# Performance work log

Measured on AMD Instinct MI355X. Metric: run time of the kernel, lower is better.

The kernel has to match this reference:

```python
import jax, jax.numpy as jnp
import numpy as np

B, C, H, W = 4, 256, 48, 48
KD, NH, AR = 32, 8, 4
D = AR * KD            # 128, value dim per head
NHKD = NH * KD         # 256
DH = NH * D            # 1024
EPS = 1e-5


def _bn(y, g, b):
    # BN with fresh running stats (mean=0, var=1): y*g/sqrt(1+eps)+b, over channel dim
    s = g / jnp.sqrt(jnp.float32(1.0) + EPS)
    return y * s[None, :, None] + b[None, :, None]


def setup_inputs() -> dict:
    key = jax.random.key(0)
    ks = jax.random.split(key, 13)
    w = lambda k, sh: jax.random.normal(k, sh, jnp.float32) * 0.05
    g = lambda k, sh: 1.0 + jax.random.normal(k, sh, jnp.float32) * 0.05
    return {
        "x": jax.random.normal(ks[0], (B, C, H, W), jnp.float32),
        "wq": w(ks[1], (NHKD, C)), "gq": g(ks[2], (NHKD,)), "bq": w(ks[3], (NHKD,)),
        "wk": w(ks[4], (NHKD, C)), "gk": g(ks[5], (NHKD,)), "bk": w(ks[6], (NHKD,)),
        "wv": w(ks[7], (DH, C)),   "gv": g(ks[8], (DH,)),   "bv": w(ks[9], (DH,)),
        "wp": w(ks[10], (C, DH)),  "gp": g(ks[11], (C,)),   "bp": w(ks[12], (C,)),
    }


def reference(x, wq, gq, bq, wk, gk, bk, wv, gv, bv, wp, gp, bp):
    b, c, h, w = x.shape
    n = h * w
    xf = x.reshape(b, c, n)                                   # [B,C,N]
    # 1x1 conv == channel matmul, then BN
    q = _bn(jnp.einsum('oc,bcn->bon', wq, xf), gq, bq).reshape(b, NH, KD, n)
    k = _bn(jnp.einsum('oc,bcn->bon', wk, xf), gk, bk).reshape(b, NH, KD, n)
    v = _bn(jnp.einsum('oc,bcn->bon', wv, xf), gv, bv).reshape(b, NH, D, n)
    # NOTE: original forward does NOT apply self.scale
    attn = jax.nn.softmax(jnp.einsum('bhkn,bhkm->bhnm', q, k), axis=-1)  # [B,H,N,N]
    xx = jnp.einsum('bhnm,bhdm->bhdn', attn, v).reshape(b, DH, n)        # [B,DH,N]
    out = _bn(jnp.einsum('oc,bcn->bon', wp, jax.nn.relu(xx)), gp, bp)
    return out.reshape(b, c, h, w)
```

## Files before the change

kernel.cpp:

```cpp
#include <hip/hip_runtime.h>

#define BB 4
#define C 256
#define HW 2304
#define NH 8
#define KD 32
#define D 128
#define DH 1024
#define MQ 256

typedef unsigned short bf16u;
typedef __attribute__((ext_vector_type(8))) short short8;
typedef __attribute__((ext_vector_type(4))) float f32x4;
typedef __attribute__((ext_vector_type(4))) unsigned ux4;
typedef __attribute__((ext_vector_type(2))) unsigned ux2;

union U8 { ux4 u; short8 s; };

__device__ __forceinline__ bf16u f2b(float f) {
    unsigned u = __float_as_uint(f);
    return (bf16u)((u + 0x7fffu + ((u >> 16) & 1u)) >> 16);
}
__device__ __forceinline__ unsigned pkb(float a, float b) {
    return __builtin_amdgcn_perm(__float_as_uint(b) + 0x8000u,
                                 __float_as_uint(a) + 0x8000u, 0x07060302u);
}

__device__ __forceinline__ void glds16(const bf16u* g, bf16u* l) {
    __builtin_amdgcn_global_load_lds(
        (const __attribute__((address_space(1))) unsigned int*)g,
        (__attribute__((address_space(3))) unsigned int*)l,
        16, 0, 0);
}

#define MFMA32 __builtin_amdgcn_mfma_f32_16x16x32_bf16

__global__ __launch_bounds__(256) void prepx(
    const float* __restrict__ wq, const float* __restrict__ wk, const float* __restrict__ wv,
    const float* __restrict__ gq, const float* __restrict__ bq,
    const float* __restrict__ gk, const float* __restrict__ bk,
    const float* __restrict__ gv, const float* __restrict__ bv,
    const float* __restrict__ x,
    bf16u* __restrict__ WcT, float* __restrict__ biasc, bf16u* __restrict__ xT)
{
    __shared__ float tile[64][68];
    const float rs = rsqrtf(1.0f + 1e-5f);
    const float L2E = 1.4426950408889634f;
    const int t = threadIdx.x, blk = blockIdx.x;
    if (blk < 192) {
        const int idx = (blk*256 + t) * 8;
        const int row = idx >> 8;
        const int k   = idx & 255;
        const float* src; float sc;
        if (row < 256)      { src = wq + idx;            sc = gq[row]*rs*L2E; }
        else if (row < 512) { src = wk + (idx - 65536);  sc = gk[row-256]*rs; }
        else                { src = wv + (idx - 131072); sc = gv[row-512]*rs; }
        float4 a = *(const float4*)(src);
        float4 c = *(const float4*)(src + 4);
        ux4 v;
        v.x = pkb(a.x*sc, a.y*sc); v.y = pkb(a.z*sc, a.w*sc);
        v.z = pkb(c.x*sc, c.y*sc); v.w = pkb(c.z*sc, c.w*sc);
        const size_t dst = (size_t)((row>>7)*8 + (k>>5))*4096
                         + (size_t)((row&127)*4 + ((k&31)>>3))*8;
        *(ux4*)(WcT + dst) = v;
    } else if (blk == 192) {
        #pragma unroll
        for (int kk = 0; kk < 6; ++kk) {
            const int r = kk*256 + t;
            float v;
            if (r < 256)      v = bq[r] * L2E;
            else if (r < 512) v = bk[r - 256];
            else              v = bv[r - 512];
            biasc[r] = v;
        }
    } else {
        const int idx = blk - 193;
        const int c0 = (idx & 3) * 64, n0 = ((idx >> 2) % 36) * 64, b = idx / 144;
        const float* xb = x + (size_t)b * C * HW;
        #pragma unroll
        for (int rr = 0; rr < 4; ++rr) {
            const int cl = rr*16 + (t >> 4);
            float4 v = *(const float4*)(xb + (size_t)(c0 + cl) * HW + n0 + (t & 15)*4);
            tile[cl][(t&15)*4+0] = v.x; tile[cl][(t&15)*4+1] = v.y;
            tile[cl][(t&15)*4+2] = v.z; tile[cl][(t&15)*4+3] = v.w;
        }
        __syncthreads();
        const int nl = t >> 2, ch = t & 3;
        short8 v0, v1;
        #pragma unroll
        for (int kk = 0; kk < 8; ++kk) v0[kk] = (short)f2b(tile[ch*16+kk][nl]);
        #pragma unroll
        for (int kk = 0; kk < 8; ++kk) v1[kk] = (short)f2b(tile[ch*16+8+kk][nl]);
        bf16u* dst = xT + ((size_t)b*HW + n0 + nl) * C + c0 + ch*16;
        *(short8*)(dst)     = v0;
        *(short8*)(dst + 8) = v1;
    }
}

__global__ __launch_bounds__(256, 3) void qkv_gemm(
    const bf16u* __restrict__ WcT, const float* __restrict__ biasc,
    const bf16u* __restrict__ xT,
    bf16u* __restrict__ qT, bf16u* __restrict__ kT, bf16u* __restrict__ vO)
{
    const int mt = blockIdx.x, ntb = blockIdx.y, b = blockIdx.z;
    const int r0 = mt * 128, c0 = ntb * 128;
    const int t = threadIdx.x, w = t >> 6, l = t & 63;
    const int l15 = l & 15, q = l >> 4;
    const int wr = w >> 1, wc = w & 1;

    __shared__ bf16u smem[24576];

    const bf16u* xb = xT + (size_t)b * HW * C;

    const int sA0 = w*128 + l, sA1 = w*128 + 64 + l;
    const bf16u* gA0 = WcT + (size_t)mt*32768 + (size_t)sA0*8;
    const bf16u* gA1 = WcT + (size_t)mt*32768 + (size_t)sA1*8;
    const bf16u* gB0 = xb + (size_t)(c0 + (sA0>>2)) * C + (sA0&3)*8;
    const bf16u* gB1 = xb + (size_t)(c0 + (sA1>>2)) * C + (sA1&3)*8;

    f32x4 acc[4][4];
    #pragma unroll
    for (int i = 0; i < 4; ++i)
        #pragma unroll
        for (int j = 0; j < 4; ++j) { acc[i][j][0]=0.f; acc[i][j][1]=0.f; acc[i][j][2]=0.f; acc[i][j][3]=0.f; }

    auto stage = [&](int it2, int bb) {
        bf16u* As = smem + bb*4096;
        bf16u* Bs = smem + 12288 + bb*4096;
        glds16(gA0 + it2*4096, As + sA0*8);
        glds16(gA1 + it2*4096, As + sA1*8);
        glds16(gB0 + it2*32,   Bs + sA0*8);
        glds16(gB1 + it2*32,   Bs + sA1*8);
    };

    const bool isV = (r0 >= 512);
    stage(0, 0); stage(1, 1);
    for (int it = 0; it < 8; ++it) {
        __syncthreads();
        if (it + 2 < 8) stage(it + 2, (it + 2) % 3);
        const bf16u* A = smem + (it % 3) * 4096;
        const bf16u* B = smem + 12288 + (it % 3) * 4096;
        short8 af[4], bf[4];
        #pragma unroll
        for (int i = 0; i < 4; ++i) af[i] = *(const short8*)(A + (wr*64 + i*16 + l15)*32 + q*8);
        #pragma unroll
        for (int j = 0; j < 4; ++j) bf[j] = *(const short8*)(B + (wc*64 + j*16 + l15)*32 + q*8);
        if (!isV) {
            #pragma unroll
            for (int i = 0; i < 4; ++i)
                #pragma unroll
                for (int j = 0; j < 4; ++j)
                    acc[i][j] = MFMA32(af[i], bf[j], acc[i][j], 0, 0, 0);
        } else {
            #pragma unroll
            for (int i = 0; i < 4; ++i)
                #pragma unroll
                for (int j = 0; j < 4; ++j)
                    acc[i][j] = MFMA32(bf[j], af[i], acc[i][j], 0, 0, 0);
        }
    }

    __syncthreads();
    bf16u* Od = smem + w * 4608;

    if (!isV) {
        float bC[4][4];
        #pragma unroll
        for (int i = 0; i < 4; ++i)
            #pragma unroll
            for (int r = 0; r < 4; ++r)
                bC[i][r] = biasc[r0 + wr*64 + i*16 + q*4 + r];
        #pragma unroll
        for (int i = 0; i < 4; ++i)
            #pragma unroll
            for (int j = 0; j < 4; ++j) {
                float y0 = acc[i][j][0] + bC[i][0];
                float y1 = acc[i][j][1] + bC[i][1];
                float y2 = acc[i][j][2] + bC[i][2];
                float y3 = acc[i][j][3] + bC[i][3];
                ux2 pk; pk.x = pkb(y0, y1); pk.y = pkb(y2, y3);
                *(ux2*)(Od + (j*16 + l15)*72 + i*16 + q*4) = pk;
            }
        bf16u* dst = (r0 < 256) ? qT : kT;
        #pragma unroll
        for (int hh = 0; hh < 2; ++hh) {
            const int h = ((r0 & 255) + wr*64 + hh*32) >> 5;
            bf16u* dh_ = dst + (size_t)(b*NH + h) * HW * KD;
            #pragma unroll
            for (int rg = 0; rg < 4; ++rg) {
                const int row = rg*16 + (l >> 2);
                const int n = c0 + wc*64 + row;
                short8 v = *(const short8*)(Od + row*72 + hh*32 + (l & 3)*8);
                *(short8*)(dh_ + (size_t)n * KD + (l & 3)*8) = v;
            }
        }
    } else {
        float bC[4];
        #pragma unroll
        for (int i = 0; i < 4; ++i)
            bC[i] = biasc[r0 + wr*64 + i*16 + l15];
        #pragma unroll
        for (int i = 0; i < 4; ++i)
            #pragma unroll
            for (int j = 0; j < 4; ++j) {
                float y0 = acc[i][j][0] + bC[i];
                float y1 = acc[i][j][1] + bC[i];
                float y2 = acc[i][j][2] + bC[i];
                float y3 = acc[i][j][3] + bC[i];
                ux2 pk; pk.x = pkb(y0, y1); pk.y = pkb(y2, y3);
                const int p = (j >> 1)*32 + q*8 + (j & 1)*4;
                *(ux2*)(Od + (i*16 + l15)*72 + p) = pk;
            }
        bf16u* dst = vO + (size_t)b * DH * HW;
        #pragma unroll
        for (int it2 = 0; it2 < 8; ++it2) {
            const int row = it2*8 + (l >> 3);
            const int d = (r0 - 512) + wr*64 + row;
            short8 v = *(const short8*)(Od + row*72 + (l & 7)*8);
            *(short8*)(dst + (size_t)d * HW + c0 + wc*64 + (l & 7)*8) = v;
        }
    }
}

__global__ __launch_bounds__(128, 2) void attn_mfma(
    const bf16u* __restrict__ qT, const bf16u* __restrict__ kT,
    const bf16u* __restrict__ vg, bf16u* __restrict__ xg)
{
    const int nt = blockIdx.x, h = blockIdx.y, b = blockIdx.z;
    const int n0 = nt * 96;
    const int t = threadIdx.x;
    const int w = t >> 6, l = t & 63, l15 = l & 15, q = l >> 4;

    const bf16u* qTh = qT + (size_t)(b*NH + h) * HW * KD;
    const bf16u* kTh = kT + (size_t)(b*NH + h) * HW * KD;
    const bf16u* vh  = vg + ((size_t)b*DH + (size_t)h*D) * HW;

    __shared__ bf16u smem[16384];

    short8 qf[3];
    #pragma unroll
    for (int g = 0; g < 3; ++g)
        qf[g] = *(const short8*)(qTh + (size_t)(n0 + w*48 + g*16 + l15) * KD + q*8);

    const short8 ones = { (short)0x3F80, (short)0x3F80, (short)0x3F80, (short)0x3F80,
                          (short)0x3F80, (short)0x3F80, (short)0x3F80, (short)0x3F80 };

    f32x4 o[3][8];
    #pragma unroll
    for (int g = 0; g < 3; ++g)
        #pragma unroll
        for (int d = 0; d < 8; ++d) { o[g][d][0]=0.f; o[g][d][1]=0.f; o[g][d][2]=0.f; o[g][d][3]=0.f; }
    f32x4 os[3];
    #pragma unroll
    for (int g = 0; g < 3; ++g) { os[g][0]=0.f; os[g][1]=0.f; os[g][2]=0.f; os[g][3]=0.f; }
    const f32x4 zero = {0.f, 0.f, 0.f, 0.f};

    auto stageV = [&](int m0, int bb) {
        bf16u* Vs = smem + bb*8192;
        #pragma unroll
        for (int j = 0; j < 8; ++j) {
            const int s = (w*8 + j)*64 + l;
            const int d = s >> 3, c = s & 7, cg = c ^ (d & 7);
            glds16(vh + (size_t)d*HW + m0 + cg*8, Vs + (w*8 + j)*512);
        }
    };

    short8 kfc[4];
    #pragma unroll
    for (int kt = 0; kt < 4; ++kt)
        kfc[kt] = *(const short8*)(kTh + (size_t)(kt*16 + l15) * KD + q*8);
    stageV(0, 0);

    for (int mt = 0; mt < 36; ++mt) {
        __syncthreads();
        if (mt < 35) stageV((mt+1)*64, (mt+1)&1);
        const bf16u* Vs = smem + (mt&1)*8192;

        unsigned dA[3][4], dB[3][4];
        #pragma unroll
        for (int g = 0; g < 3; ++g) {
            f32x4 st[4];
            #pragma unroll
            for (int kt = 0; kt < 4; ++kt)
                st[kt] = MFMA32(kfc[kt], qf[g], zero, 0, 0, 0);
            #pragma unroll
            for (int kt = 0; kt < 4; ++kt) {
                float p0 = __builtin_amdgcn_exp2f(st[kt][0]);
                float p1 = __builtin_amdgcn_exp2f(st[kt][1]);
                float p2 = __builtin_amdgcn_exp2f(st[kt][2]);
                float p3 = __builtin_amdgcn_exp2f(st[kt][3]);
                dA[g][kt] = pkb(p0, p1); dB[g][kt] = pkb(p2, p3);
            }
        }

        if (mt < 35) {
            #pragma unroll
            for (int kt = 0; kt < 4; ++kt)
                kfc[kt] = *(const short8*)(kTh + (size_t)((mt+1)*64 + kt*16 + l15) * KD + q*8);
        }

        #pragma unroll
        for (int kh = 0; kh < 2; ++kh) {
            U8 u[3];
            #pragma unroll
            for (int g = 0; g < 3; ++g) {
                u[g].u[0] = dA[g][kh*2];   u[g].u[1] = dB[g][kh*2];
                u[g].u[2] = dA[g][kh*2+1]; u[g].u[3] = dB[g][kh*2+1];
            }
            #pragma unroll
            for (int dt = 0; dt < 8; ++dt) {
                const int d = dt*16 + l15;
                short8 vf = *(const short8*)(Vs + d*64 + (((kh*4 + q) ^ (d & 7)) * 8));
                #pragma unroll
                for (int g = 0; g < 3; ++g)
                    o[g][dt] = MFMA32(u[g].s, vf, o[g][dt], 0, 0, 0);
            }
            #pragma unroll
            for (int g = 0; g < 3; ++g)
                os[g] = MFMA32(u[g].s, ones, os[g], 0, 0, 0);
        }
    }

    float inv[3][4];
    #pragma unroll
    for (int g = 0; g < 3; ++g)
        #pragma unroll
        for (int r = 0; r < 4; ++r)
            inv[g][r] = 1.0f / os[g][r];
    __syncthreads();
    bf16u* Od = smem + w * 6528;
    #pragma unroll
    for (int g = 0; g < 3; ++g)
        #pragma unroll
        for (int dt = 0; dt < 8; ++dt)
            #pragma unroll
            for (int r = 0; r < 4; ++r) {
                float v = fmaxf(o[g][dt][r] * inv[g][r], 0.f);
                Od[(g*16 + q*4 + r)*136 + dt*16 + l15] = f2b(v);
            }
    bf16u* xb = xg + ((size_t)b*HW + n0 + w*48) * DH + h*D;
    #pragma unroll
    for (int it = 0; it < 6; ++it) {
        const int row = it*8 + (l >> 3);
        #pragma unroll
        for (int hf = 0; hf < 2; ++hf) {
            const int ch = hf*8 + (l & 7);
            *(short8*)(xb + (size_t)row*DH + ch*8) =
                *(const short8*)(Od + row*136 + ch*8);
        }
    }
}

__global__ __launch_bounds__(256) void prep2(
    const float* __restrict__ wp, const float* __restrict__ gp,
    bf16u* __restrict__ WpT)
{
    const float rs = rsqrtf(1.0f + 1e-5f);
    const int item = blockIdx.x*256 + threadIdx.x;
    const int row = item >> 7;
    const int k   = (item & 127) * 8;
    const float sc = gp[row] * rs;
    const float* src = wp + (size_t)row*DH + k;
    float4 a = *(const float4*)(src);
    float4 c = *(const float4*)(src + 4);
    ux4 v;
    v.x = pkb(a.x*sc, a.y*sc); v.y = pkb(a.z*sc, a.w*sc);
    v.z = pkb(c.x*sc, c.y*sc); v.w = pkb(c.z*sc, c.w*sc);
    const size_t dst = (size_t)((row>>4)*32 + (k>>5))*512
                     + (size_t)(((k>>3)&3)*16 + (row&15))*8;
    *(ux4*)(WpT + dst) = v;
}

__global__ __launch_bounds__(256, 3) void out_gemm(
    const bf16u* __restrict__ WpT, const float* __restrict__ bp,
    const bf16u* __restrict__ xx, float* __restrict__ out)
{
    const int mt = blockIdx.x, ntb = blockIdx.y, b = blockIdx.z;
    const int r0 = mt * 64, c0 = ntb * 64;
    const int t = threadIdx.x, w = t >> 6, l = t & 63;
    const int l15 = l & 15, q = l >> 4;
    const int wr = w >> 1, wc = w & 1;

    __shared__ bf16u smem[12288];

    const bf16u* xb = xx + (size_t)b * HW * DH;

    const int sB0 = w*128 + l, sB1 = w*128 + 64 + l;
    const bf16u* gB0 = xb + (size_t)(c0 + (sB0>>3)) * DH + (sB0&7)*8;
    const bf16u* gB1 = xb + (size_t)(c0 + (sB1>>3)) * DH + (sB1&7)*8;
    const bf16u* gA  = WpT + (size_t)(mt*4 + wr*2)*32*512 + (size_t)l*8;

    f32x4 acc[2][2];
    #pragma unroll
    for (int i = 0; i < 2; ++i)
        #pragma unroll
        for (int j = 0; j < 2; ++j) { acc[i][j][0]=0.f; acc[i][j][1]=0.f; acc[i][j][2]=0.f; acc[i][j][3]=0.f; }

    auto stage = [&](int it2, int bb) {
        bf16u* Bs = smem + bb*4096;
        glds16(gB0 + it2*64, Bs + sB0*8);
        glds16(gB1 + it2*64, Bs + sB1*8);
    };

    stage(0, 0); stage(1, 1);
    for (int it = 0; it < 16; ++it) {
        __syncthreads();
        if (it + 2 < 16) stage(it + 2, (it + 2) % 3);
        const bf16u* B = smem + (it % 3) * 4096;
        #pragma unroll
        for (int kk = 0; kk < 2; ++kk) {
            short8 af[2], bf[2];
            #pragma unroll
            for (int i = 0; i < 2; ++i)
                af[i] = *(const short8*)(gA + (size_t)(i*32 + it*2 + kk)*512);
            #pragma unroll
            for (int j = 0; j < 2; ++j)
                bf[j] = *(const short8*)(B + (wc*32 + j*16 + l15)*64 + kk*32 + q*8);
            #pragma unroll
            for (int i = 0; i < 2; ++i)
                #pragma unroll
                for (int j = 0; j < 2; ++j)
                    acc[i][j] = MFMA32(af[i], bf[j], acc[i][j], 0, 0, 0);
        }
    }

    #pragma unroll
    for (int i = 0; i < 2; ++i)
        #pragma unroll
        for (int r = 0; r < 4; ++r) {
            const int oc = r0 + wr*32 + i*16 + q*4 + r;
            const float bi = bp[oc];
            #pragma unroll
            for (int j = 0; j < 2; ++j) {
                const int n = c0 + wc*32 + j*16 + l15;
                out[((size_t)b*C + oc)*HW + n] = acc[i][j][r] + bi;
            }
        }
}

extern "C" void kernel_launch(void* const* d_in, const int* in_sizes, int n_in,
                              void* d_out, int out_size, void* d_ws, size_t ws_size,
                              hipStream_t stream) {
    const float* x  = (const float*)d_in[0];
    const float* wq = (const float*)d_in[1];
    const float* gq = (const float*)d_in[2];
    const float* bq = (const float*)d_in[3];
    const float* wk = (const float*)d_in[4];
    const float* gk = (const float*)d_in[5];
    const float* bk = (const float*)d_in[6];
    const float* wv = (const float*)d_in[7];
    const float* gv = (const float*)d_in[8];
    const float* bv = (const float*)d_in[9];
    const float* wp = (const float*)d_in[10];
    const float* gp = (const float*)d_in[11];
    const float* bp = (const float*)d_in[12];
    float* out = (float*)d_out;

    bf16u* qw = (bf16u*)d_ws;
    bf16u* kw = qw + (size_t)BB * MQ * HW;
    bf16u* vw = kw + (size_t)BB * MQ * HW;
    bf16u* xw = vw + (size_t)BB * DH * HW;
    bf16u* xTb = xw;
    bf16u* WcT = xw + (size_t)BB * MQ * HW;
    float* biasc = (float*)(WcT + 393216);
    bf16u* WpT = qw;

    hipLaunchKernelGGL(prepx, dim3(769), dim3(256), 0, stream,
                       wq, wk, wv, gq, bq, gk, bk, gv, bv, x, WcT, biasc, xTb);
    hipLaunchKernelGGL(qkv_gemm, dim3(12, 18, BB), dim3(256), 0, stream,
                       WcT, biasc, xTb, qw, kw, vw);
    hipLaunchKernelGGL(attn_mfma, dim3(24, NH, BB), dim3(128), 0, stream,
                       qw, kw, vw, xw);
    hipLaunchKernelGGL(prep2, dim3(128), dim3(256), 0, stream, wp, gp, WpT);
    hipLaunchKernelGGL(out_gemm, dim3(4, 36, BB), dim3(256), 0, stream,
                       WpT, bp, xw, out);
}
```

Baseline: 192.4 us.

## Store V in MFMA-fragment tiled layout and load half of V directly to registers

The projection kernel now writes V in a per-head, per-64-key tile layout where each 16-byte fragment lines up with the MFMA B-operand. The attention kernel stages only half the d rows of V into LDS through the async global-to-LDS path. The other half is loaded straight from global memory into registers, which cuts LDS size and LDS read traffic. The cost is more live registers and global loads that sit on the critical path and are not prefetched.

```diff
diff --git a/kernel.cpp b/kernel.cpp
--- a/kernel.cpp
+++ b/kernel.cpp
@@ -211,13 +211,17 @@
                 const int p = (j >> 1)*32 + q*8 + (j & 1)*4;
                 *(ux2*)(Od + (i*16 + l15)*72 + p) = pk;
             }
-        bf16u* dst = vO + (size_t)b * DH * HW;
+        const int h  = mt - 4;
+        const int nt = (c0 >> 6) + wc;
+        bf16u* base = vO + (((size_t)(b*NH + h)*36 + nt)*2) * 4096;
+        const int kh  = (l & 7) >> 2;
+        const int sub = ((l & 7) & 3) * 8;
         #pragma unroll
         for (int it2 = 0; it2 < 8; ++it2) {
             const int row = it2*8 + (l >> 3);
-            const int d = (r0 - 512) + wr*64 + row;
+            const int dh = wr*64 + row;
             short8 v = *(const short8*)(Od + row*72 + (l & 7)*8);
-            *(short8*)(dst + (size_t)d * HW + c0 + wc*64 + (l & 7)*8) = v;
+            *(short8*)(base + (size_t)kh*4096 + dh*32 + sub) = v;
         }
     }
 }
@@ -233,9 +237,9 @@
 
     const bf16u* qTh = qT + (size_t)(b*NH + h) * HW * KD;
     const bf16u* kTh = kT + (size_t)(b*NH + h) * HW * KD;
-    const bf16u* vh  = vg + ((size_t)b*DH + (size_t)h*D) * HW;
-
-    __shared__ bf16u smem[16384];
+    const bf16u* vh  = vg + (size_t)(b*NH + h) * 36 * 8192;
+
+    __shared__ bf16u smem[13056];
 
     short8 qf[3];
     #pragma unroll
@@ -255,13 +259,14 @@
     for (int g = 0; g < 3; ++g) { os[g][0]=0.f; os[g][1]=0.f; os[g][2]=0.f; os[g][3]=0.f; }
     const f32x4 zero = {0.f, 0.f, 0.f, 0.f};
 
-    auto stageV = [&](int m0, int bb) {
-        bf16u* Vs = smem + bb*8192;
-        #pragma unroll
-        for (int j = 0; j < 8; ++j) {
-            const int s = (w*8 + j)*64 + l;
+    auto stageV = [&](int mt_, int bb) {
+        const bf16u* tb = vh + (size_t)mt_ * 8192;
+        bf16u* Vs = smem + bb*4096;
+        #pragma unroll
+        for (int j = 0; j < 4; ++j) {
+            const int s = (w*4 + j)*64 + l;
             const int d = s >> 3, c = s & 7, cg = c ^ (d & 7);
-            glds16(vh + (size_t)d*HW + m0 + cg*8, Vs + (w*8 + j)*512);
+            glds16(tb + (cg >> 2)*4096 + d*32 + (cg & 3)*8, Vs + (w*4 + j)*512);
         }
     };
 
@@ -273,8 +278,16 @@
 
     for (int mt = 0; mt < 36; ++mt) {
         __syncthreads();
-        if (mt < 35) stageV((mt+1)*64, (mt+1)&1);
-        const bf16u* Vs = smem + (mt&1)*8192;
+        if (mt < 35) stageV(mt + 1, (mt+1)&1);
+        const bf16u* Vs = smem + (mt&1)*4096;
+        const bf16u* tb = vh + (size_t)mt * 8192;
+
+        short8 vdir[2][4];
+        #pragma unroll
+        for (int kh = 0; kh < 2; ++kh)
+            #pragma unroll
+            for (int dt2 = 0; dt2 < 4; ++dt2)
+                vdir[kh][dt2] = *(const short8*)(tb + kh*4096 + (64 + dt2*16 + l15)*32 + q*8);
 
         unsigned dA[3][4], dB[3][4];
         #pragma unroll
@@ -308,12 +321,18 @@
                 u[g].u[2] = dA[g][kh*2+1]; u[g].u[3] = dB[g][kh*2+1];
             }
             #pragma unroll
-            for (int dt = 0; dt < 8; ++dt) {
+            for (int dt = 0; dt < 4; ++dt) {
                 const int d = dt*16 + l15;
                 short8 vf = *(const short8*)(Vs + d*64 + (((kh*4 + q) ^ (d & 7)) * 8));
                 #pragma unroll
                 for (int g = 0; g < 3; ++g)
                     o[g][dt] = MFMA32(u[g].s, vf, o[g][dt], 0, 0, 0);
+            }
+            #pragma unroll
+            for (int dt2 = 0; dt2 < 4; ++dt2) {
+                #pragma unroll
+                for (int g = 0; g < 3; ++g)
+                    o[g][4 + dt2] = MFMA32(u[g].s, vdir[kh][dt2], o[g][4 + dt2], 0, 0, 0);
             }
             #pragma unroll
             for (int g = 0; g < 3; ++g)
```

New measurement: 212.5 us. +10.5%, slower.
